# Optimization experiments

Measured on AMD Instinct MI355X. Metric: run time of the kernel, lower is better.

## Reference

```python
import jax, jax.numpy as jnp
import numpy as np

H = 64  # hidden size

def setup_inputs() -> dict:
    key = jax.random.key(0)
    ks = jax.random.split(key, 7)
    B, T = 256, 5000
    s = 1.0 / np.sqrt(H)  # PyTorch LSTM init scale
    return {
        "x":    jax.random.normal(ks[0], (B, T), dtype=jnp.float32),
        "W_ih": jax.random.uniform(ks[1], (4 * H, 1), jnp.float32, -s, s),
        "W_hh": jax.random.uniform(ks[2], (4 * H, H), jnp.float32, -s, s),
        "b_ih": jax.random.uniform(ks[3], (4 * H,), jnp.float32, -s, s),
        "b_hh": jax.random.uniform(ks[4], (4 * H,), jnp.float32, -s, s),
        "W_fc": jax.random.uniform(ks[5], (128, H), jnp.float32, -s, s),
        "b_fc": jax.random.uniform(ks[6], (128,), jnp.float32, -s, s),
    }

def _lstm_last_hidden(x, W_ih, W_hh, b_ih, b_hh):
    # x: [B, T]; returns last hidden state h_T: [B, H]
    B, T = x.shape
    # input projection for all timesteps at once: [B, T, 4H]
    # (input_size == 1, so this is an outer product with W_ih[:, 0])
    x_proj = x[:, :, None] * W_ih[:, 0][None, None, :] + (b_ih + b_hh)

    def step(carry, xp_t):
        h, c = carry
        gates = xp_t + h @ W_hh.T  # [B, 4H]
        i = jax.nn.sigmoid(gates[:, 0 * H:1 * H])
        f = jax.nn.sigmoid(gates[:, 1 * H:2 * H])
        g = jnp.tanh(gates[:, 2 * H:3 * H])
        o = jax.nn.sigmoid(gates[:, 3 * H:4 * H])
        c = f * c + i * g
        h = o * jnp.tanh(c)
        return (h, c), None

    h0 = jnp.zeros((B, H), x.dtype)
    c0 = jnp.zeros((B, H), x.dtype)
    (h, c), _ = jax.lax.scan(step, (h0, c0), jnp.swapaxes(x_proj, 0, 1))
    return h

def reference(x, W_ih, W_hh, b_ih, b_hh, W_fc, b_fc):
    h_last = _lstm_last_hidden(x, W_ih, W_hh, b_ih, b_hh)  # [B, H]
    return jax.nn.relu(h_last @ W_fc.T + b_fc)  # [B, 128]
```

## Files before the change

### kernel.cpp

```cpp
#include <hip/hip_runtime.h>


#define LSTM_H 64
#define LSTM_T 5000
#define LSTM_B 256

typedef float v2f __attribute__((ext_vector_type(2)));

__device__ __forceinline__ void pk_fma_acc(v2f& acc, v2f a, v2f b) {
    asm("v_pk_fma_f32 %0, %1, %2, %0" : "+v"(acc) : "v"(a), "v"(b));
}

__device__ __forceinline__ float fast_rcp(float v) {
    return __builtin_amdgcn_rcpf(v);
}

__global__ __launch_bounds__(256, 1) void ECGLSTM_lstm_fused(
    const float* __restrict__ x,
    const float* __restrict__ W_ih,
    const float* __restrict__ W_hh,
    const float* __restrict__ b_ih,
    const float* __restrict__ b_hh,
    const float* __restrict__ W_fc,
    const float* __restrict__ b_fc,
    float* __restrict__ out)
{
    const int tid  = threadIdx.x;
    const int lane = tid & 63;
    const int b    = blockIdx.x;

    __shared__ float xch[LSTM_T];
    __shared__ float hbuf[2][LSTM_H];
    __shared__ float gbuf[2][4 * LSTM_H];

    const float* xb = x + b * LSTM_T;
    for (int i = tid; i < LSTM_T; i += 256) xch[i] = xb[i];

    v2f w[LSTM_H / 2];
    {
        const float4* wrow = reinterpret_cast<const float4*>(W_hh + tid * LSTM_H);
        #pragma unroll
        for (int i = 0; i < LSTM_H / 4; ++i) {
            float4 v = wrow[i];
            w[2 * i]     = v2f{v.x, v.y};
            w[2 * i + 1] = v2f{v.z, v.w};
        }
    }
    const float wih  = W_ih[tid];
    const float bias = b_ih[tid] + b_hh[tid];
    const bool  is_tanh = ((tid >> 6) == 2);

    float c = 0.0f;
    hbuf[0][lane] = 0.0f;
    __syncthreads();

    #define LSTM_STEP(t, P)                                                    \
    {                                                                          \
        const float xv = xch[(t)];                          \
        v2f A = {0.f, 0.f}, C = {0.f, 0.f};                                    \
        const float4* h4 = reinterpret_cast<const float4*>(hbuf[(P)]);         \
        _Pragma("unroll")                                                      \
        for (int i = 0; i < LSTM_H / 4; ++i) {                                 \
            float4 hv = h4[i];                             \
            pk_fma_acc(A, v2f{hv.x, hv.y}, w[2 * i]);                          \
            pk_fma_acc(C, v2f{hv.z, hv.w}, w[2 * i + 1]);                      \
        }                                                                      \
        float g = fmaf(xv, wih, bias) + ((A.x + A.y) + (C.x + C.y));           \
        float act;                                                             \
        if (is_tanh) {                                                         \
            float e = __expf(2.0f * g);                                        \
            act = 1.0f - 2.0f * fast_rcp(e + 1.0f);                            \
        } else {                                                               \
            float e = __expf(-g);                                              \
            act = fast_rcp(1.0f + e);                                          \
        }                                                                      \
        gbuf[(P)][tid] = act;                                                  \
        __syncthreads();                                  \
        const float ig = gbuf[(P)][lane];                                      \
        const float fg = gbuf[(P)][LSTM_H + lane];                             \
        const float gg = gbuf[(P)][2 * LSTM_H + lane];                         \
        const float og = gbuf[(P)][3 * LSTM_H + lane];                         \
        c = fmaf(fg, c, ig * gg);                                              \
        float e2 = __expf(2.0f * c);                                           \
        float th = 1.0f - 2.0f * fast_rcp(e2 + 1.0f);                          \
        hbuf[1 - (P)][lane] = og * th;                    \
    }

    for (int t = 0; t < LSTM_T; t += 2) {
        LSTM_STEP(t, 0);
        LSTM_STEP(t + 1, 1);
    }
    #undef LSTM_STEP

    if (tid < 128) {
        float s = b_fc[tid];
        const float4* wf = reinterpret_cast<const float4*>(W_fc + tid * LSTM_H);
        const float4* h4 = reinterpret_cast<const float4*>(hbuf[0]);
        #pragma unroll
        for (int i = 0; i < LSTM_H / 4; ++i) {
            float4 wv = wf[i];
            float4 hv = h4[i];
            s = fmaf(hv.x, wv.x, s);
            s = fmaf(hv.y, wv.y, s);
            s = fmaf(hv.z, wv.z, s);
            s = fmaf(hv.w, wv.w, s);
        }
        out[b * 128 + tid] = fmaxf(s, 0.0f);
    }
}

extern "C" void kernel_launch(void* const* d_in, const int* in_sizes, int n_in,
                              void* d_out, int out_size, void* d_ws, size_t ws_size,
                              hipStream_t stream) {
    const float* x    = (const float*)d_in[0];
    const float* W_ih = (const float*)d_in[1];
    const float* W_hh = (const float*)d_in[2];
    const float* b_ih = (const float*)d_in[3];
    const float* b_hh = (const float*)d_in[4];
    const float* W_fc = (const float*)d_in[5];
    const float* b_fc = (const float*)d_in[6];
    float* out = (float*)d_out;

    ECGLSTM_lstm_fused<<<LSTM_B, 256, 0, stream>>>(
        x, W_ih, W_hh, b_ih, b_hh, W_fc, b_fc, out);
}
```

Baseline: 2.095 ms.

## Process two batch rows per block to interleave independent LSTM recurrences

```diff
diff --git a/kernel.cpp b/kernel.cpp
--- a/kernel.cpp
+++ b/kernel.cpp
@@ -4,6 +4,8 @@
 #define LSTM_H 64
 #define LSTM_T 5000
 #define LSTM_B 256
+#define NB     2
+#define NBLK   (LSTM_B / NB)
 
 typedef float v2f __attribute__((ext_vector_type(2)));
 
@@ -27,14 +29,17 @@
 {
     const int tid  = threadIdx.x;
     const int lane = tid & 63;
-    const int b    = blockIdx.x;
+    const int b0   = blockIdx.x * NB;
 
-    __shared__ float xch[LSTM_T];
-    __shared__ float hbuf[2][LSTM_H];
-    __shared__ float gbuf[2][4 * LSTM_H];
+    __shared__ float xch[NB][LSTM_T];
+    __shared__ float hbuf[NB][2][LSTM_H];
+    __shared__ float gbuf[NB][2][4 * LSTM_H];
 
-    const float* xb = x + b * LSTM_T;
-    for (int i = tid; i < LSTM_T; i += 256) xch[i] = xb[i];
+    #pragma unroll
+    for (int nb = 0; nb < NB; ++nb) {
+        const float* xb = x + (b0 + nb) * LSTM_T;
+        for (int i = tid; i < LSTM_T; i += 256) xch[nb][i] = xb[i];
+    }
 
     v2f w[LSTM_H / 2];
     {
@@ -46,44 +51,73 @@
             w[2 * i + 1] = v2f{v.z, v.w};
         }
     }
-    const float wih  = W_ih[tid];
-    const float bias = b_ih[tid] + b_hh[tid];
-    const bool  is_tanh = ((tid >> 6) == 2);
+    #pragma unroll
+    for (int i = 0; i < LSTM_H / 2; ++i) asm volatile("" : "+v"(w[i]));
 
-    float c = 0.0f;
-    hbuf[0][lane] = 0.0f;
+    float wih  = W_ih[tid];
+    float bias = b_ih[tid] + b_hh[tid];
+    asm volatile("" : "+v"(wih), "+v"(bias));
+    const bool is_tanh = ((tid >> 6) == 2);
+
+    float cA = 0.0f, cB = 0.0f;
+    hbuf[0][0][lane] = 0.0f;
+    hbuf[1][0][lane] = 0.0f;
     __syncthreads();
 
     #define LSTM_STEP(t, P)                                                    \
     {                                                                          \
-        const float xv = xch[(t)];                          \
-        v2f A = {0.f, 0.f}, C = {0.f, 0.f};                                    \
-        const float4* h4 = reinterpret_cast<const float4*>(hbuf[(P)]);         \
+        const float xvA = xch[0][(t)];                                         \
+        const float xvB = xch[1][(t)];                                         \
+        v2f AA = {0.f,0.f}, CA = {0.f,0.f};                                    \
+        v2f AB = {0.f,0.f}, CB = {0.f,0.f};                                    \
+        const float4* hA = reinterpret_cast<const float4*>(hbuf[0][(P)]);      \
+        const float4* hB = reinterpret_cast<const float4*>(hbuf[1][(P)]);      \
         _Pragma("unroll")                                                      \
         for (int i = 0; i < LSTM_H / 4; ++i) {                                 \
-            float4 hv = h4[i];                             \
-            pk_fma_acc(A, v2f{hv.x, hv.y}, w[2 * i]);                          \
-            pk_fma_acc(C, v2f{hv.z, hv.w}, w[2 * i + 1]);                      \
+            float4 ha = hA[i];                             \
+            float4 hb = hB[i];                                                 \
+            pk_fma_acc(AA, v2f{ha.x, ha.y}, w[2 * i]);                         \
+            pk_fma_acc(CA, v2f{ha.z, ha.w}, w[2 * i + 1]);                     \
+            pk_fma_acc(AB, v2f{hb.x, hb.y}, w[2 * i]);                         \
+            pk_fma_acc(CB, v2f{hb.z, hb.w}, w[2 * i + 1]);                     \
         }                                                                      \
-        float g = fmaf(xv, wih, bias) + ((A.x + A.y) + (C.x + C.y));           \
-        float act;                                                             \
+        float gA = fmaf(xvA, wih, bias) + ((AA.x + AA.y) + (CA.x + CA.y));     \
+        float gB = fmaf(xvB, wih, bias) + ((AB.x + AB.y) + (CB.x + CB.y));     \
+        float actA, actB;                                                      \
         if (is_tanh) {                                                         \
-            float e = __expf(2.0f * g);                                        \
-            act = 1.0f - 2.0f * fast_rcp(e + 1.0f);                            \
+            float eA = __expf(2.0f * gA);                                      \
+            actA = 1.0f - 2.0f * fast_rcp(eA + 1.0f);                          \
+            float eB = __expf(2.0f * gB);                                      \
+            actB = 1.0f - 2.0f * fast_rcp(eB + 1.0f);                          \
         } else {                                                               \
-            float e = __expf(-g);                                              \
-            act = fast_rcp(1.0f + e);                                          \
+            float eA = __expf(-gA);                                            \
+            actA = fast_rcp(1.0f + eA);                                        \
+            float eB = __expf(-gB);                                            \
+            actB = fast_rcp(1.0f + eB);                                        \
         }                                                                      \
-        gbuf[(P)][tid] = act;                                                  \
+        gbuf[0][(P)][tid] = actA;                                              \
+        gbuf[1][(P)][tid] = actB;                                              \
         __syncthreads();                                  \
-        const float ig = gbuf[(P)][lane];                                      \
-        const float fg = gbuf[(P)][LSTM_H + lane];                             \
-        const float gg = gbuf[(P)][2 * LSTM_H + lane];                         \
-        const float og = gbuf[(P)][3 * LSTM_H + lane];                         \
-        c = fmaf(fg, c, ig * gg);                                              \
-        float e2 = __expf(2.0f * c);                                           \
-        float th = 1.0f - 2.0f * fast_rcp(e2 + 1.0f);                          \
-        hbuf[1 - (P)][lane] = og * th;                    \
+        {                                                                      \
+            const float ig = gbuf[0][(P)][lane];                               \
+            const float fg = gbuf[0][(P)][LSTM_H + lane];                      \
+            const float gg = gbuf[0][(P)][2 * LSTM_H + lane];                  \
+            const float og = gbuf[0][(P)][3 * LSTM_H + lane];                  \
+            cA = fmaf(fg, cA, ig * gg);                                        \
+            float e2 = __expf(2.0f * cA);                                      \
+            float th = 1.0f - 2.0f * fast_rcp(e2 + 1.0f);                      \
+            hbuf[0][1 - (P)][lane] = og * th;             \
+        }                                                                      \
+        {                                                                      \
+            const float ig = gbuf[1][(P)][lane];                               \
+            const float fg = gbuf[1][(P)][LSTM_H + lane];                      \
+            const float gg = gbuf[1][(P)][2 * LSTM_H + lane];                  \
+            const float og = gbuf[1][(P)][3 * LSTM_H + lane];                  \
+            cB = fmaf(fg, cB, ig * gg);                                        \
+            float e2 = __expf(2.0f * cB);                                      \
+            float th = 1.0f - 2.0f * fast_rcp(e2 + 1.0f);                      \
+            hbuf[1][1 - (P)][lane] = og * th;                                  \
+        }                                                                      \
     }
 
     for (int t = 0; t < LSTM_T; t += 2) {
@@ -93,19 +127,25 @@
     #undef LSTM_STEP
 
     if (tid < 128) {
-        float s = b_fc[tid];
         const float4* wf = reinterpret_cast<const float4*>(W_fc + tid * LSTM_H);
-        const float4* h4 = reinterpret_cast<const float4*>(hbuf[0]);
+        float4 wv[LSTM_H / 4];
         #pragma unroll
-        for (int i = 0; i < LSTM_H / 4; ++i) {
-            float4 wv = wf[i];
-            float4 hv = h4[i];
-            s = fmaf(hv.x, wv.x, s);
-            s = fmaf(hv.y, wv.y, s);
-            s = fmaf(hv.z, wv.z, s);
-            s = fmaf(hv.w, wv.w, s);
+        for (int i = 0; i < LSTM_H / 4; ++i) wv[i] = wf[i];
+        const float bf = b_fc[tid];
+        #pragma unroll
+        for (int nb = 0; nb < NB; ++nb) {
+            float s = bf;
+            const float4* h4 = reinterpret_cast<const float4*>(hbuf[nb][0]);
+            #pragma unroll
+            for (int i = 0; i < LSTM_H / 4; ++i) {
+                float4 hv = h4[i];
+                s = fmaf(hv.x, wv[i].x, s);
+                s = fmaf(hv.y, wv[i].y, s);
+                s = fmaf(hv.z, wv[i].z, s);
+                s = fmaf(hv.w, wv[i].w, s);
+            }
+            out[(b0 + nb) * 128 + tid] = fmaxf(s, 0.0f);
         }
-        out[b * 128 + tid] = fmaxf(s, 0.0f);
     }
 }
 
@@ -121,6 +161,6 @@
     const float* b_fc = (const float*)d_in[6];
     float* out = (float*)d_out;
 
-    ECGLSTM_lstm_fused<<<LSTM_B, 256, 0, stream>>>(
+    ECGLSTM_lstm_fused<<<NBLK, 256, 0, stream>>>(
         x, W_ih, W_hh, b_ih, b_hh, W_fc, b_fc, out);
 }
```

New measurement: 3.387 ms. 61.7% more time.
